# Kernel tuning notes

Measured on AMD Instinct MI355X. Metric: run time of the kernel, lower is better.

## Reference

```python
import jax, jax.numpy as jnp
import numpy as np

B, S, D, H, L, K = 16, 384, 512, 8, 4, 7
HD = D // H
MAXLEN = 400


def _pos_encoding(d=D, max_len=MAXLEN):
    # Faithful to the (unusual) torch loop: even idx i -> sin(pos/10000**(2i/d)),
    # odd idx i+1 -> cos(pos/10000**(2(i+1)/d))
    pe = np.zeros((max_len, d), dtype=np.float32)
    pos = np.arange(max_len, dtype=np.float64)[:, None]
    i = np.arange(0, d, 2)
    pe[:, i] = np.sin(pos / 10000.0 ** (2 * i / d))
    pe[:, i + 1] = np.cos(pos / 10000.0 ** (2 * (i + 1) / d))
    return jnp.asarray(pe)

POS_ENC = _pos_encoding()


def layer_norm(x, g, b, eps=1e-5):
    m = jnp.mean(x, -1, keepdims=True)
    v = jnp.mean((x - m) ** 2, -1, keepdims=True)
    return (x - m) * jax.lax.rsqrt(v + eps) * g + b


def dsconv(x, dw_w, pw_w, pw_b):
    # x: [B,S,D]; depthwise conv1d (no bias) then pointwise 1x1 (bias)
    xc = jnp.transpose(x, (0, 2, 1))  # [B,D,S]
    y = jax.lax.conv_general_dilated(
        xc, dw_w, window_strides=(1,), padding=[(K // 2, K // 2)],
        dimension_numbers=("NCH", "OIH", "NCH"), feature_group_count=D)  # [B,D,S]
    return jnp.einsum("bcs,oc->bso", y, pw_w) + pw_b  # [B,S,D]


def setup_inputs():
    key = jax.random.key(0)
    ks = jax.random.split(key, 16)
    sc = 0.02
    inp = {
        "x": jax.random.normal(ks[0], (B, S, D), jnp.float32),
        "mask": jax.random.randint(ks[1], (B, S), 0, 2, jnp.int32),
        "dw_w": jax.random.normal(ks[2], (L, D, 1, K), jnp.float32) * sc,
        "pw_w": jax.random.normal(ks[3], (L, D, D), jnp.float32) * sc,
        "pw_b": jnp.zeros((L, D), jnp.float32),
        "conv_ln_g": jnp.ones((L, D), jnp.float32),
        "conv_ln_b": jnp.zeros((L, D), jnp.float32),
        "pos_ln_g": jnp.ones((D,), jnp.float32),
        "pos_ln_b": jnp.zeros((D,), jnp.float32),
        "wq": jax.random.normal(ks[4], (D, D), jnp.float32) * sc,
        "bq": jnp.zeros((D,), jnp.float32),
        "wk": jax.random.normal(ks[5], (D, D), jnp.float32) * sc,
        "bk": jnp.zeros((D,), jnp.float32),
        "wv": jax.random.normal(ks[6], (D, D), jnp.float32) * sc,
        "bv": jnp.zeros((D,), jnp.float32),
        "wo": jax.random.normal(ks[7], (D, D), jnp.float32) * sc,
        "bo": jnp.zeros((D,), jnp.float32),
        "ff_ln_g": jnp.ones((D,), jnp.float32),
        "ff_ln_b": jnp.zeros((D,), jnp.float32),
        "ff_w": jax.random.normal(ks[8], (D, D), jnp.float32) * sc,
        "ff_b": jnp.zeros((D,), jnp.float32),
    }
    return inp


def attention(x, mask, wq, bq, wk, bk, wv, bv, wo, bo):
    def heads(w, b):
        y = jnp.einsum("bsd,od->bso", x, w) + b
        return jnp.transpose(y.reshape(B, S, H, HD), (0, 2, 1, 3))  # [B,H,S,HD]
    q, k, v = heads(wq, bq), heads(wk, bk), heads(wv, bv)
    energy = jnp.einsum("bhqd,bhkd->bhqk", q, k) / jnp.sqrt(jnp.float32(HD))
    m = (mask == 1)[:, None, None, :]  # [B,1,1,S]
    energy = jnp.where(m, jnp.float32(-1e10), energy)
    alpha = jax.nn.softmax(energy, axis=-1)  # dropout = identity (eval)
    a = jnp.einsum("bhqk,bhkd->bhqd", alpha, v)
    a = jnp.transpose(a, (0, 2, 1, 3)).reshape(B, S, D)
    return jnp.einsum("bsd,od->bso", a, wo) + bo


def reference(x, mask, dw_w, pw_w, pw_b, conv_ln_g, conv_ln_b, pos_ln_g, pos_ln_b,
              wq, bq, wk, bk, wv, bv, wo, bo, ff_ln_g, ff_ln_b, ff_w, ff_b):
    out = x + POS_ENC[None, :S, :]
    res = out
    out = layer_norm(out, pos_ln_g, pos_ln_b)
    for i in range(L):
        out = jax.nn.relu(dsconv(out, dw_w[i], pw_w[i], pw_b[i]))
        out = out + res  # dropout = identity (eval)
        res = out
        out = layer_norm(out, conv_ln_g[i], conv_ln_b[i])
    out = attention(out, mask, wq, bq, wk, bk, wv, bv, wo, bo)
    out = out + res
    res = out
    out = layer_norm(out, ff_ln_g, ff_ln_b)
    out = jax.nn.relu(jnp.einsum("bsd,od->bso", out, ff_w) + ff_b)
    return out + res
```

## Files before the change

### kernel.cpp

```cpp
#include <hip/hip_runtime.h>

#define BB 16
#define SS 384
#define DD 512
#define HH 8
#define HDIM 64
#define LLAY 4
#define KW 7
#define MM (BB*SS)

typedef unsigned short u16;
typedef unsigned int u32;
typedef short short8v __attribute__((ext_vector_type(8)));
typedef short short4v __attribute__((ext_vector_type(4)));
typedef float floatx4 __attribute__((ext_vector_type(4)));

__device__ __forceinline__ float bf2f(u16 u) {
    union { u32 i; float f; } v; v.i = ((u32)u) << 16; return v.f;
}
__device__ __forceinline__ u16 f2bf(float f) {
    union { float f; u32 i; } v; v.f = f;
    return (u16)((v.i + 0x7FFFu + ((v.i >> 16) & 1u)) >> 16);
}
__device__ __forceinline__ bool sniff_f32(const void* dtp) {
    return *((const u32*)dtp) == 0x3F800000u;
}
__device__ __forceinline__ float ldf(const void* p, long i, bool f32) {
    return f32 ? ((const float*)p)[i] : bf2f(((const u16*)p)[i]);
}
__device__ __forceinline__ short8v ldfrag_scalar(const void* p, long i, bool f32) {
    short8v r;
    if (f32) {
        const float* q = (const float*)p + i;
#pragma unroll
        for (int j = 0; j < 8; j++) r[j] = (short)f2bf(q[j]);
    } else {
        r = *(const short8v*)((const u16*)p + i);
    }
    return r;
}

__device__ __forceinline__ void load_lds16(const u16* g, u16* l) {
    __builtin_amdgcn_global_load_lds((const __attribute__((address_space(1))) void*)g,
                                     (__attribute__((address_space(3))) void*)l, 16, 0, 0);
}
__device__ __forceinline__ int swz(int row) { return (row & 3) ^ ((row >> 2) & 3); }
__device__ __forceinline__ short8v lds_frag(const u16* buf, int row, int quad) {
    return *(const short8v*)(buf + ((size_t)row * 4 + (quad ^ swz(row))) * 8);
}

#define WCV_DW 2359296
#define WCV_TOT (WCV_DW + LLAY*KW*DD)
#define NCVB ((WCV_TOT + 255) / 256)

__global__ __launch_bounds__(256) void posln_cvt_kernel(
    const void* __restrict__ x, const void* __restrict__ g, const void* __restrict__ bvec,
    u16* __restrict__ res, u16* __restrict__ out,
    const void* __restrict__ pw_w, const void* __restrict__ wq,
    const void* __restrict__ wk, const void* __restrict__ wv,
    const void* __restrict__ wo, const void* __restrict__ ff_w,
    const void* __restrict__ dw_w, u16* __restrict__ wdst,
    const void* __restrict__ dtp) {
    const bool f32 = sniff_f32(dtp);
    const int tid = threadIdx.x;
    if (blockIdx.x >= MM) {
        const int i = (blockIdx.x - MM) * 256 + tid;
        if (i >= WCV_TOT) return;
        const void* src; long idx;
        if (i < 1048576) { src = pw_w; idx = i; }
        else if (i < WCV_DW) {
            const int j = i - 1048576;
            const int m = j >> 18;
            idx = j & 262143;
            src = (m == 0) ? wq : (m == 1) ? wk : (m == 2) ? wv : (m == 3) ? wo : ff_w;
        } else {
            const int j = i - WCV_DW;
            const int l = j / (KW * DD);
            const int r1 = j % (KW * DD);
            const int t = r1 / DD, c = r1 % DD;
            src = dw_w; idx = ((long)l * DD + c) * KW + t;
        }
        wdst[i] = f2bf(ldf(src, idx, f32));
        return;
    }
    const int row = blockIdx.x;
    const int s = row % SS;
    float v[2];
#pragma unroll
    for (int i = 0; i < 2; i++) {
        const int d = tid + i * 256;
        const float freq = __expf(-(float)d * 0.035977892078032f);
        const float arg = (float)s * freq;
        const float pe = (d & 1) ? __cosf(arg) : __sinf(arg);
        v[i] = ldf(x, (long)row * DD + d, f32) + pe;
        res[row * DD + d] = f2bf(v[i]);
    }
    float sum = v[0] + v[1], sq = v[0] * v[0] + v[1] * v[1];
#pragma unroll
    for (int off = 32; off; off >>= 1) { sum += __shfl_down(sum, off); sq += __shfl_down(sq, off); }
    __shared__ float red[4][2];
    const int wv2 = tid >> 6;
    if ((tid & 63) == 0) { red[wv2][0] = sum; red[wv2][1] = sq; }
    __syncthreads();
    sum = red[0][0] + red[1][0] + red[2][0] + red[3][0];
    sq  = red[0][1] + red[1][1] + red[2][1] + red[3][1];
    const float mean = sum * (1.f / DD);
    const float rstd = rsqrtf(sq * (1.f / DD) - mean * mean + 1e-5f);
#pragma unroll
    for (int i = 0; i < 2; i++) {
        const int d = tid + i * 256;
        out[row * DD + d] = f2bf((v[i] - mean) * rstd * ldf(g, d, f32) + ldf(bvec, d, f32));
    }
}

__global__ __launch_bounds__(512) void lnres_kernel(const u16* __restrict__ y,
                                                    const void* __restrict__ g,
                                                    const void* __restrict__ bvec,
                                                    int blayer,
                                                    u16* __restrict__ out,
                                                    const void* __restrict__ dtp) {
    const bool f32 = sniff_f32(dtp);
    const long voff = (long)blayer * DD;
    const int row = blockIdx.x * 8 + (threadIdx.x >> 6);
    const int lane = threadIdx.x & 63;
    const short8v v = *(const short8v*)(y + (size_t)row * DD + lane * 8);
    float f[8], sum = 0.f, sq = 0.f;
#pragma unroll
    for (int j = 0; j < 8; j++) { f[j] = bf2f((u16)v[j]); sum += f[j]; sq += f[j] * f[j]; }
#pragma unroll
    for (int off = 32; off; off >>= 1) { sum += __shfl_xor(sum, off); sq += __shfl_xor(sq, off); }
    const float mean = sum * (1.f / DD);
    const float rstd = rsqrtf(sq * (1.f / DD) - mean * mean + 1e-5f);
    short8v o;
#pragma unroll
    for (int j = 0; j < 8; j++) {
        const int d = lane * 8 + j;
        o[j] = (short)f2bf((f[j] - mean) * rstd * ldf(g, voff + d, f32) + ldf(bvec, voff + d, f32));
    }
    *(short8v*)(out + (size_t)row * DD + lane * 8) = o;
}

template <int VEC>
__global__ __launch_bounds__(256) void dwconv_kernel(const u16* __restrict__ in,
                                                     const void* __restrict__ w, int layer,
                                                     u16* __restrict__ out,
                                                     const void* __restrict__ dtp) {
    if constexpr (VEC) {
        const int bsw = (blockIdx.x & 7) * (MM * DD / 8 / 256 / 8) + (blockIdx.x >> 3);
        const int idx = bsw * 256 + threadIdx.x;
        const int c8 = (idx & 63) * 8;
        const int ms = idx >> 6;
        const int s = ms % SS;
        const u16* wl = (const u16*)w + (size_t)layer * KW * DD;
        float acc[8] = {0, 0, 0, 0, 0, 0, 0, 0};
#pragma unroll
        for (int t = 0; t < KW; t++) {
            const int ss2 = s + t - 3;
            if (ss2 >= 0 && ss2 < SS) {
                const short8v iv = *(const short8v*)(in + (size_t)(ms + t - 3) * DD + c8);
                const short8v wv = *(const short8v*)(wl + t * DD + c8);
#pragma unroll
                for (int j = 0; j < 8; j++)
                    acc[j] += bf2f((u16)iv[j]) * bf2f((u16)wv[j]);
            }
        }
        short8v ov;
#pragma unroll
        for (int j = 0; j < 8; j++) ov[j] = (short)f2bf(acc[j]);
        *(short8v*)(out + (size_t)ms * DD + c8) = ov;
    } else {
        const bool f32 = sniff_f32(dtp);
        const long woff = (long)layer * DD * KW;
        const int idx = blockIdx.x * 256 + threadIdx.x;
        const int c = idx & (DD - 1);
        const int ms = idx >> 9;
        const int s = ms % SS;
        float acc = 0.f;
#pragma unroll
        for (int t = 0; t < KW; t++) {
            const int ss2 = s + t - 3;
            if (ss2 >= 0 && ss2 < SS)
                acc += bf2f(in[(ms + t - 3) * DD + c]) * ldf(w, woff + c * KW + t, f32);
        }
        out[idx] = f2bf(acc);
    }
}

__device__ __forceinline__ void stage64(const u16* A, const u16* Wp, int m0,
                                        u16* Ab, u16* Wb, int tid, int k0) {
#pragma unroll
    for (int j = 0; j < 2; j++) {
        const int c = j * 256 + tid;
        const int row = c >> 2;
        const int kp = (c & 3) ^ swz(row);
        load_lds16(Wp + (size_t)row * DD + k0 + kp * 8, Wb + (size_t)c * 8);
    }
    {
        const int row = tid >> 2;
        const int kp = (tid & 3) ^ swz(row);
        load_lds16(A + (size_t)(m0 + row) * DD + k0 + kp * 8, Ab + (size_t)tid * 8);
    }
}

__device__ __forceinline__ floatx4 mfma16(short8v a, short8v b, floatx4 c) {
    return __builtin_amdgcn_mfma_f32_16x16x32_bf16(a, b, c, 0, 0, 0);
}

__device__ __forceinline__ void kloop64(const u16* A, const u16* Wp, int m0,
                                        u16* Abuf, u16* Wbuf,
                                        int tid, int wm, int wn, int ln15, int quad,
                                        floatx4 acc[2][4]) {
    stage64(A, Wp, m0, Abuf, Wbuf, tid, 0);
    __syncthreads();
    for (int ks = 0; ks < 16; ks++) {
        const int cur = ks & 1;
        u16* Ab = Abuf + cur * (64 * 32);
        u16* Wb = Wbuf + cur * (128 * 32);
        if (ks < 15)
            stage64(A, Wp, m0, Abuf + (cur ^ 1) * (64 * 32),
                    Wbuf + (cur ^ 1) * (128 * 32), tid, (ks + 1) * 32);
        const short8v a0 = lds_frag(Ab, wm * 32 + ln15, quad);
        const short8v a1 = lds_frag(Ab, wm * 32 + 16 + ln15, quad);
#pragma unroll
        for (int nt = 0; nt < 4; nt++) {
            const short8v b = lds_frag(Wb, wn * 64 + nt * 16 + ln15, quad);
            acc[0][nt] = mfma16(a0, b, acc[0][nt]);
            acc[1][nt] = mfma16(a1, b, acc[1][nt]);
        }
        __syncthreads();
    }
}

template <int RELU, int FINAL>
__global__ __launch_bounds__(256, 4) void gemm64_kernel(
    const u16* __restrict__ A, const u16* __restrict__ W,
    const void* __restrict__ bias, int blayer,
    const u16* __restrict__ res_in, u16* __restrict__ res_out,
    void* __restrict__ out, const void* __restrict__ dtp) {
    const bool f32 = sniff_f32(dtp);
    const long voff = (long)blayer * DD;
    __shared__ __align__(16) u16 smem[12288];
    u16* Wbuf = smem;
    u16* Abuf = smem + 8192;
    const int tid = threadIdx.x;
    const int m0 = blockIdx.x * 64, n0 = blockIdx.y * 128;
    const int wave = tid >> 6, lane = tid & 63;
    const int wm = wave >> 1, wn = wave & 1;
    const int ln15 = lane & 15, quad = lane >> 4;

    floatx4 acc[2][4];
#pragma unroll
    for (int mt = 0; mt < 2; mt++)
#pragma unroll
        for (int nt = 0; nt < 4; nt++) acc[mt][nt] = {0.f, 0.f, 0.f, 0.f};

    kloop64(A, W + (size_t)n0 * DD, m0, Abuf, Wbuf, tid, wm, wn, ln15, quad, acc);

#pragma unroll
    for (int nt = 0; nt < 4; nt++) {
        const int col = n0 + wn * 64 + nt * 16 + ln15;
        const float bval = ldf(bias, voff + col, f32);
#pragma unroll
        for (int mt = 0; mt < 2; mt++)
#pragma unroll
            for (int r = 0; r < 4; r++) {
                const int m = m0 + wm * 32 + mt * 16 + quad * 4 + r;
                float y = acc[mt][nt][r] + bval;
                if (RELU) y = fmaxf(y, 0.f);
                y += bf2f(res_in[(size_t)m * DD + col]);
                if (res_out) res_out[(size_t)m * DD + col] = f2bf(y);
                if constexpr (FINAL) {
                    if (f32) ((float*)out)[(size_t)m * DD + col] = y;
                    else     ((u16*)out)[(size_t)m * DD + col] = f2bf(y);
                }
            }
    }
}

#define VP 72
__global__ __launch_bounds__(256, 4) void qkv64_kernel(
    const u16* __restrict__ A,
    const u16* __restrict__ Wq, const u16* __restrict__ Wk, const u16* __restrict__ Wv,
    const void* __restrict__ bq, const void* __restrict__ bk, const void* __restrict__ bv,
    u16* __restrict__ qo, u16* __restrict__ ko, u16* __restrict__ vo,
    const void* __restrict__ dtp) {
    const bool f32 = sniff_f32(dtp);
    const int sel = blockIdx.z;
    const u16* W = (sel == 0) ? Wq : (sel == 1) ? Wk : Wv;
    const void* bias = (sel == 0) ? bq : (sel == 1) ? bk : bv;

    __shared__ __align__(16) u16 smem[12288];
    u16* Wbuf = smem;
    u16* Abuf = smem + 8192;
    u16 (*vtile)[VP] = (u16 (*)[VP])smem;

    const int tid = threadIdx.x;
    const int m0 = blockIdx.x * 64, n0 = blockIdx.y * 128;
    const int wave = tid >> 6, lane = tid & 63;
    const int wm = wave >> 1, wn = wave & 1;
    const int ln15 = lane & 15, quad = lane >> 4;
    const int bidx = m0 / SS;

    floatx4 acc[2][4];
#pragma unroll
    for (int mt = 0; mt < 2; mt++)
#pragma unroll
        for (int nt = 0; nt < 4; nt++) acc[mt][nt] = {0.f, 0.f, 0.f, 0.f};

    kloop64(A, W + (size_t)n0 * DD, m0, Abuf, Wbuf, tid, wm, wn, ln15, quad, acc);

    if (sel == 2) {
#pragma unroll
        for (int nt = 0; nt < 4; nt++) {
            const int cl = wn * 64 + nt * 16 + ln15;
            const float bval = ldf(bias, n0 + cl, f32);
#pragma unroll
            for (int mt = 0; mt < 2; mt++)
#pragma unroll
                for (int r = 0; r < 4; r++)
                    vtile[cl][wm * 32 + mt * 16 + quad * 4 + r] = f2bf(acc[mt][nt][r] + bval);
        }
        __syncthreads();
        const int c = tid & 127, half = tid >> 7;
        const int col = n0 + c;
        const int h = col >> 6, hd = col & 63;
        u16* dst = vo + ((size_t)(bidx * HH + h) * HDIM + hd) * SS
                      + (m0 - bidx * SS) + half * 32;
        const u16* srcl = &vtile[c][half * 32];
#pragma unroll
        for (int j = 0; j < 4; j++)
            *(short8v*)(dst + j * 8) = *(const short8v*)(srcl + j * 8);
    } else {
        u16* out = (sel == 0) ? qo : ko;
#pragma unroll
        for (int nt = 0; nt < 4; nt++) {
            const int col = n0 + wn * 64 + nt * 16 + ln15;
            const int h = col >> 6, hd = col & 63;
            const float bval = ldf(bias, col, f32);
#pragma unroll
            for (int mt = 0; mt < 2; mt++)
#pragma unroll
                for (int r = 0; r < 4; r++) {
                    const int m = m0 + wm * 32 + mt * 16 + quad * 4 + r;
                    const int s = m - bidx * SS;
                    out[((size_t)(bidx * HH + h) * SS + s) * HDIM + hd] = f2bf(acc[mt][nt][r] + bval);
                }
        }
    }
}

template <int RELU, int DO_LN, int FINAL>
__global__ __launch_bounds__(512, 4) void gemm16_kernel(
    const u16* __restrict__ A, const void* __restrict__ W, int wlayer,
    const void* __restrict__ bias, const void* __restrict__ g,
    const void* __restrict__ bvec, int blayer,
    const u16* __restrict__ res_in, u16* __restrict__ res_out,
    void* __restrict__ out, const void* __restrict__ dtp) {
    const bool f32 = sniff_f32(dtp);
    const long woff = (long)wlayer * DD * DD;
    const long voff = (long)blayer * DD;
    __shared__ float part[8][16][2];
    const int tid = threadIdx.x;
    const int m0 = blockIdx.x * 16;
    const int wave = tid >> 6, lane = tid & 63;
    const int ln15 = lane & 15, quad = lane >> 4;

    floatx4 acc[4];
#pragma unroll
    for (int nt = 0; nt < 4; nt++) acc[nt] = {0.f, 0.f, 0.f, 0.f};

    const u16* A0 = A + (size_t)(m0 + ln15) * DD + quad * 8;
#pragma unroll
    for (int ks = 0; ks < 16; ks++) {
        const int k0 = ks * 32;
        short8v a0 = *(const short8v*)(A0 + k0);
        short8v b[4];
#pragma unroll
        for (int nt = 0; nt < 4; nt++) {
            const long wrow = woff + (long)(wave * 64 + nt * 16 + ln15) * DD + quad * 8 + k0;
            b[nt] = ldfrag_scalar(W, wrow, f32);
        }
#pragma unroll
        for (int nt = 0; nt < 4; nt++)
            acc[nt] = mfma16(a0, b[nt], acc[nt]);
    }

#pragma unroll
    for (int nt = 0; nt < 4; nt++) {
        const int col = wave * 64 + nt * 16 + ln15;
        const float bval = ldf(bias, voff + col, f32);
#pragma unroll
        for (int r = 0; r < 4; r++) {
            const int m = m0 + quad * 4 + r;
            float y = acc[nt][r] + bval;
            if (RELU) y = fmaxf(y, 0.f);
            y += bf2f(res_in[(size_t)m * DD + col]);
            if (res_out) res_out[(size_t)m * DD + col] = f2bf(y);
            acc[nt][r] = y;
        }
    }
    if constexpr (DO_LN) {
        float ls[4], lq[4];
#pragma unroll
        for (int r = 0; r < 4; r++) {
            float s = 0.f, q = 0.f;
#pragma unroll
            for (int nt = 0; nt < 4; nt++) { const float y = acc[nt][r]; s += y; q += y * y; }
            ls[r] = s; lq[r] = q;
        }
#pragma unroll
        for (int off = 1; off < 16; off <<= 1)
#pragma unroll
            for (int r = 0; r < 4; r++) {
                ls[r] += __shfl_xor(ls[r], off);
                lq[r] += __shfl_xor(lq[r], off);
            }
        if (ln15 == 0) {
#pragma unroll
            for (int r = 0; r < 4; r++) {
                part[wave][quad * 4 + r][0] = ls[r];
                part[wave][quad * 4 + r][1] = lq[r];
            }
        }
        __syncthreads();
        float mean[4], rstd[4];
#pragma unroll
        for (int r = 0; r < 4; r++) {
            const int rr = quad * 4 + r;
            float s = 0.f, q = 0.f;
#pragma unroll
            for (int wv = 0; wv < 8; wv++) { s += part[wv][rr][0]; q += part[wv][rr][1]; }
            const float mn = s * (1.f / DD);
            mean[r] = mn;
            rstd[r] = rsqrtf(q * (1.f / DD) - mn * mn + 1e-5f);
        }
#pragma unroll
        for (int nt = 0; nt < 4; nt++) {
            const int col = wave * 64 + nt * 16 + ln15;
            const float gv = ldf(g, voff + col, f32);
            const float bv = ldf(bvec, voff + col, f32);
#pragma unroll
            for (int r = 0; r < 4; r++) {
                const int m = m0 + quad * 4 + r;
                ((u16*)out)[(size_t)m * DD + col] =
                    f2bf((acc[nt][r] - mean[r]) * rstd[r] * gv + bv);
            }
        }
    } else {
#pragma unroll
        for (int nt = 0; nt < 4; nt++) {
            const int col = wave * 64 + nt * 16 + ln15;
#pragma unroll
            for (int r = 0; r < 4; r++) {
                const int m = m0 + quad * 4 + r;
                if (FINAL && f32) ((float*)out)[(size_t)m * DD + col] = acc[nt][r];
                else              ((u16*)out)[(size_t)m * DD + col] = f2bf(acc[nt][r]);
            }
        }
    }
}

__global__ __launch_bounds__(512, 4) void qkv16_kernel(
    const u16* __restrict__ A,
    const void* __restrict__ Wq, const void* __restrict__ Wk, const void* __restrict__ Wv,
    const void* __restrict__ bq, const void* __restrict__ bk, const void* __restrict__ bv,
    u16* __restrict__ qo, u16* __restrict__ ko, u16* __restrict__ vo,
    const void* __restrict__ dtp) {
    const bool f32 = sniff_f32(dtp);
    const int sel = blockIdx.y;
    const void* W = (sel == 0) ? Wq : (sel == 1) ? Wk : Wv;
    const void* bias = (sel == 0) ? bq : (sel == 1) ? bk : bv;

    const int tid = threadIdx.x;
    const int m0 = blockIdx.x * 16;
    const int wave = tid >> 6, lane = tid & 63;
    const int ln15 = lane & 15, quad = lane >> 4;
    const int bidx = m0 / SS;

    floatx4 acc[4];
#pragma unroll
    for (int nt = 0; nt < 4; nt++) acc[nt] = {0.f, 0.f, 0.f, 0.f};

    const u16* A0 = A + (size_t)(m0 + ln15) * DD + quad * 8;
#pragma unroll
    for (int ks = 0; ks < 16; ks++) {
        const int k0 = ks * 32;
        short8v a0 = *(const short8v*)(A0 + k0);
        short8v b[4];
#pragma unroll
        for (int nt = 0; nt < 4; nt++) {
            const long wrow = (long)(wave * 64 + nt * 16 + ln15) * DD + quad * 8 + k0;
            b[nt] = ldfrag_scalar(W, wrow, f32);
        }
#pragma unroll
        for (int nt = 0; nt < 4; nt++)
            acc[nt] = mfma16(a0, b[nt], acc[nt]);
    }

    if (sel == 2) {
#pragma unroll
        for (int nt = 0; nt < 4; nt++) {
            const int col = wave * 64 + nt * 16 + ln15;
            const int h = col >> 6, hd = col & 63;
            const float bval = ldf(bias, col, f32);
#pragma unroll
            for (int r = 0; r < 4; r++) {
                const int m = m0 + quad * 4 + r;
                const int s = m - bidx * SS;
                vo[((size_t)(bidx * HH + h) * HDIM + hd) * SS + s] = f2bf(acc[nt][r] + bval);
            }
        }
    } else {
        u16* out = (sel == 0) ? qo : ko;
#pragma unroll
        for (int nt = 0; nt < 4; nt++) {
            const int col = wave * 64 + nt * 16 + ln15;
            const int h = col >> 6, hd = col & 63;
            const float bval = ldf(bias, col, f32);
#pragma unroll
            for (int r = 0; r < 4; r++) {
                const int m = m0 + quad * 4 + r;
                const int s = m - bidx * SS;
                out[((size_t)(bidx * HH + h) * SS + s) * HDIM + hd] = f2bf(acc[nt][r] + bval);
            }
        }
    }
}

#define SSPF 388
#define SSPH 392
__global__ __launch_bounds__(256) void attn_kernel(const u16* __restrict__ q,
                                                   const u16* __restrict__ k,
                                                   const u16* __restrict__ vT,
                                                   const int* __restrict__ mask,
                                                   u16* __restrict__ out) {
    __shared__ float sc[16 * SSPF];
    __shared__ float rsum[16];
    u16* al = (u16*)sc;

    const int n = blockIdx.x;
    const int i = n >> 3;
    const int g = (n & 7) * 16 + i / 24;
    const int qt = i % 24;
    const int h = g & 7, b = g >> 3;
    const int q0 = qt * 16;
    const int wave = threadIdx.x >> 6, lane = threadIdx.x & 63;
    const int ln15 = lane & 15, quad = lane >> 4;

    const u16* qh = q + (size_t)(b * HH + h) * SS * HDIM;
    const u16* kh = k + (size_t)(b * HH + h) * SS * HDIM;

    const short8v* arow = (const short8v*)(qh + (q0 + ln15) * HDIM + quad * 8);
    const short8v a0 = arow[0], a1 = arow[4];
#pragma unroll
    for (int t = 0; t < 6; t++) {
        const int n0 = wave * 96 + t * 16;
        const short8v* brow = (const short8v*)(kh + (n0 + ln15) * HDIM + quad * 8);
        floatx4 acc = {0.f, 0.f, 0.f, 0.f};
        __builtin_amdgcn_s_setprio(1);
        acc = mfma16(a0, brow[0], acc);
        acc = mfma16(a1, brow[4], acc);
        __builtin_amdgcn_s_setprio(0);
        const int kk = n0 + ln15;
        const bool msk = (mask[b * SS + kk] == 1);
#pragma unroll
        for (int r = 0; r < 4; r++) {
            float v = acc[r] * 0.125f;
            if (msk) v = -1e10f;
            sc[(quad * 4 + r) * SSPF + kk] = v;
        }
    }
    __syncthreads();
    const int r = threadIdx.x >> 4, cg = threadIdx.x & 15;
    float pv[24], mx = -3.0e38f;
#pragma unroll
    for (int j = 0; j < 24; j++) { pv[j] = sc[r * SSPF + cg + 16 * j]; mx = fmaxf(mx, pv[j]); }
#pragma unroll
    for (int off = 8; off; off >>= 1) mx = fmaxf(mx, __shfl_xor(mx, off, 16));
    float sum = 0.f;
#pragma unroll
    for (int j = 0; j < 24; j++) { const float p = __expf(pv[j] - mx); pv[j] = p; sum += p; }
#pragma unroll
    for (int off = 8; off; off >>= 1) sum += __shfl_xor(sum, off, 16);
    if (cg == 0) rsum[r] = sum;
    __syncthreads();
#pragma unroll
    for (int j = 0; j < 24; j++) al[r * SSPH + cg + 16 * j] = f2bf(pv[j]);
    __syncthreads();
    const u16* vh = vT + (size_t)(b * HH + h) * HDIM * SS;
    const int d0 = wave * 16;
    floatx4 acc = {0.f, 0.f, 0.f, 0.f};
    __builtin_amdgcn_s_setprio(1);
#pragma unroll
    for (int k0 = 0; k0 < SS; k0 += 32) {
        const short8v af = *(const short8v*)(al + ln15 * SSPH + k0 + quad * 8);
        const short8v bf = *(const short8v*)(vh + (d0 + ln15) * SS + k0 + quad * 8);
        acc = mfma16(af, bf, acc);
    }
    __builtin_amdgcn_s_setprio(0);
#pragma unroll
    for (int rr = 0; rr < 4; rr++) {
        const int lr = quad * 4 + rr;
        const int s = q0 + lr;
        out[((size_t)(b * SS + s)) * DD + h * HDIM + d0 + ln15] = f2bf(acc[rr] / rsum[lr]);
    }
}

extern "C" void kernel_launch(void* const* d_in, const int* in_sizes, int n_in,
                              void* d_out, int out_size, void* d_ws, size_t ws_size,
                              hipStream_t stream) {
    (void)in_sizes; (void)n_in; (void)out_size;
    const void* x     = d_in[0];
    const int*  mask  = (const int*)d_in[1];
    const void* dw_w  = d_in[2];
    const void* pw_w  = d_in[3];
    const void* pw_b  = d_in[4];
    const void* cln_g = d_in[5];
    const void* cln_b = d_in[6];
    const void* pln_g = d_in[7];
    const void* pln_b = d_in[8];
    const void* wq    = d_in[9];
    const void* bq    = d_in[10];
    const void* wk    = d_in[11];
    const void* bk    = d_in[12];
    const void* wv    = d_in[13];
    const void* bv    = d_in[14];
    const void* wo    = d_in[15];
    const void* bo    = d_in[16];
    const void* fln_g = d_in[17];
    const void* fln_b = d_in[18];
    const void* ff_w  = d_in[19];
    const void* ff_b  = d_in[20];
    const void* dtp   = cln_g;

    const size_t nAct = (size_t)MM * DD;
    char* p = (char*)d_ws;
    u16* res   = (u16*)p; p += nAct * 2;
    u16* lnout = (u16*)p; p += nAct * 2;
    u16* tmp   = (u16*)p; p += nAct * 2;
    u16* vT    = (u16*)p; p += nAct * 2;
    u16* wcv   = (u16*)p;
    u16* kb    = (u16*)d_out;

    const size_t needFast = nAct * 2 * 4 + (size_t)WCV_TOT * 2;
    const bool fast = (ws_size >= needFast);

    if (fast) {
        posln_cvt_kernel<<<MM + NCVB, 256, 0, stream>>>(
            x, pln_g, pln_b, res, lnout,
            pw_w, wq, wk, wv, wo, ff_w, dw_w, wcv, dtp);
        const u16* w_pw = wcv;
        const u16* w_q  = wcv + 1048576;
        const u16* w_k  = wcv + 1310720;
        const u16* w_v  = wcv + 1572864;
        const u16* w_o  = wcv + 1835008;
        const u16* w_ff = wcv + 2097152;
        const u16* w_dw = wcv + WCV_DW;

        for (int i = 0; i < LLAY; i++) {
            dwconv_kernel<1><<<MM * DD / 8 / 256, 256, 0, stream>>>(lnout, w_dw, i, tmp, dtp);
            gemm64_kernel<1, 0><<<dim3(MM / 64, 4), 256, 0, stream>>>(
                tmp, w_pw + (size_t)i * DD * DD, pw_b, i, res, res, nullptr, dtp);
            lnres_kernel<<<MM / 8, 512, 0, stream>>>(res, cln_g, cln_b, i, lnout, dtp);
        }
        qkv64_kernel<<<dim3(MM / 64, 4, 3), 256, 0, stream>>>(
            lnout, w_q, w_k, w_v, bq, bk, bv, tmp, kb, vT, dtp);

        attn_kernel<<<BB * HH * (SS / 16), 256, 0, stream>>>(tmp, kb, vT, mask, lnout);

        gemm64_kernel<0, 0><<<dim3(MM / 64, 4), 256, 0, stream>>>(
            lnout, w_o, bo, 0, res, res, nullptr, dtp);
        lnres_kernel<<<MM / 8, 512, 0, stream>>>(res, fln_g, fln_b, 0, lnout, dtp);
        gemm64_kernel<1, 1><<<dim3(MM / 64, 4), 256, 0, stream>>>(
            lnout, w_ff, ff_b, 0, res, nullptr, d_out, dtp);
    } else {
        posln_cvt_kernel<<<MM, 256, 0, stream>>>(
            x, pln_g, pln_b, res, lnout,
            pw_w, wq, wk, wv, wo, ff_w, dw_w, (u16*)d_ws, dtp);
        for (int i = 0; i < LLAY; i++) {
            dwconv_kernel<0><<<MM * DD / 256, 256, 0, stream>>>(lnout, dw_w, i, tmp, dtp);
            gemm16_kernel<1, 1, 0><<<MM / 16, 512, 0, stream>>>(
                tmp, pw_w, i, pw_b, cln_g, cln_b, i, res, res, lnout, dtp);
        }
        qkv16_kernel<<<dim3(MM / 16, 3), 512, 0, stream>>>(
            lnout, wq, wk, wv, bq, bk, bv, tmp, kb, vT, dtp);

        attn_kernel<<<BB * HH * (SS / 16), 256, 0, stream>>>(tmp, kb, vT, mask, lnout);

        gemm16_kernel<0, 1, 0><<<MM / 16, 512, 0, stream>>>(
            lnout, wo, 0, bo, fln_g, fln_b, 0, res, res, lnout, dtp);
        gemm16_kernel<1, 0, 1><<<MM / 16, 512, 0, stream>>>(
            lnout, ff_w, 0, ff_b, nullptr, nullptr, 0, res, nullptr, d_out, dtp);
    }
}
```

Before: 349.4 us.

## Use 32-row GEMM tiles and per-wave 16-query attention without block syncs

Replaces the 64x128 GEMM tile with a 32x128 tile where each wave owns 32 output columns, doubling the number of blocks for the pointwise, output and FFN GEMMs. This gives more parallelism at the cost of more redundant weight loads per output. The attention kernel is restructured so each wave handles its own 16 query rows across all keys. Scores stay in registers, softmax reductions use lane shuffles, and probabilities go to a per-wave LDS slice, removing the block-wide __syncthreads and shared score buffer, with a quarter as many blocks. The trade-offs are higher register pressure (24 accumulators) and each wave rereading all of K and V.

```diff
diff --git a/kernel.cpp b/kernel.cpp
--- a/kernel.cpp
+++ b/kernel.cpp
@@ -12,7 +12,6 @@
 typedef unsigned short u16;
 typedef unsigned int u32;
 typedef short short8v __attribute__((ext_vector_type(8)));
-typedef short short4v __attribute__((ext_vector_type(4)));
 typedef float floatx4 __attribute__((ext_vector_type(4)));
 
 __device__ __forceinline__ float bf2f(u16 u) {
@@ -47,6 +46,10 @@
 __device__ __forceinline__ int swz(int row) { return (row & 3) ^ ((row >> 2) & 3); }
 __device__ __forceinline__ short8v lds_frag(const u16* buf, int row, int quad) {
     return *(const short8v*)(buf + ((size_t)row * 4 + (quad ^ swz(row))) * 8);
+}
+
+__device__ __forceinline__ floatx4 mfma16(short8v a, short8v b, floatx4 c) {
+    return __builtin_amdgcn_mfma_f32_16x16x32_bf16(a, b, c, 0, 0, 0);
 }
 
 #define WCV_DW 2359296
@@ -186,7 +189,7 @@
     }
 }
 
-__device__ __forceinline__ void stage64(const u16* A, const u16* Wp, int m0,
+__device__ __forceinline__ void stage32(const u16* A, const u16* Wp, int m0,
                                         u16* Ab, u16* Wb, int tid, int k0) {
 #pragma unroll
     for (int j = 0; j < 2; j++) {
@@ -195,15 +198,97 @@
         const int kp = (c & 3) ^ swz(row);
         load_lds16(Wp + (size_t)row * DD + k0 + kp * 8, Wb + (size_t)c * 8);
     }
+    if (tid < 128) {
+        const int row = tid >> 2;
+        const int kp = (tid & 3) ^ swz(row);
+        load_lds16(A + (size_t)(m0 + row) * DD + k0 + kp * 8, Ab + (size_t)tid * 8);
+    }
+}
+
+__device__ __forceinline__ void kloop32(const u16* A, const u16* Wp, int m0,
+                                        u16* Abuf, u16* Wbuf,
+                                        int tid, int wave, int ln15, int quad,
+                                        floatx4 acc[2][2]) {
+    stage32(A, Wp, m0, Abuf, Wbuf, tid, 0);
+    __syncthreads();
+    for (int ks = 0; ks < 16; ks++) {
+        const int cur = ks & 1;
+        u16* Ab = Abuf + cur * (32 * 32);
+        u16* Wb = Wbuf + cur * (128 * 32);
+        if (ks < 15)
+            stage32(A, Wp, m0, Abuf + (cur ^ 1) * (32 * 32),
+                    Wbuf + (cur ^ 1) * (128 * 32), tid, (ks + 1) * 32);
+        const short8v a0 = lds_frag(Ab, ln15, quad);
+        const short8v a1 = lds_frag(Ab, 16 + ln15, quad);
+#pragma unroll
+        for (int nt = 0; nt < 2; nt++) {
+            const short8v b = lds_frag(Wb, wave * 32 + nt * 16 + ln15, quad);
+            acc[0][nt] = mfma16(a0, b, acc[0][nt]);
+            acc[1][nt] = mfma16(a1, b, acc[1][nt]);
+        }
+        __syncthreads();
+    }
+}
+
+template <int RELU, int FINAL>
+__global__ __launch_bounds__(256) void gemm32w_kernel(
+    const u16* __restrict__ A, const u16* __restrict__ W,
+    const void* __restrict__ bias, int blayer,
+    const u16* __restrict__ res_in, u16* __restrict__ res_out,
+    void* __restrict__ out, const void* __restrict__ dtp) {
+    const bool f32 = sniff_f32(dtp);
+    const long voff = (long)blayer * DD;
+    __shared__ __align__(16) u16 smem[10240];
+    u16* Wbuf = smem;
+    u16* Abuf = smem + 8192;
+    const int tid = threadIdx.x;
+    const int m0 = blockIdx.x * 32, n0 = blockIdx.y * 128;
+    const int wave = tid >> 6, lane = tid & 63;
+    const int ln15 = lane & 15, quad = lane >> 4;
+
+    floatx4 acc[2][2];
+#pragma unroll
+    for (int mt = 0; mt < 2; mt++)
+#pragma unroll
+        for (int nt = 0; nt < 2; nt++) acc[mt][nt] = {0.f, 0.f, 0.f, 0.f};
+
+    kloop32(A, W + (size_t)n0 * DD, m0, Abuf, Wbuf, tid, wave, ln15, quad, acc);
+
+#pragma unroll
+    for (int nt = 0; nt < 2; nt++) {
+        const int col = n0 + wave * 32 + nt * 16 + ln15;
+        const float bval = ldf(bias, voff + col, f32);
+#pragma unroll
+        for (int mt = 0; mt < 2; mt++)
+#pragma unroll
+            for (int r = 0; r < 4; r++) {
+                const int m = m0 + mt * 16 + quad * 4 + r;
+                float y = acc[mt][nt][r] + bval;
+                if (RELU) y = fmaxf(y, 0.f);
+                y += bf2f(res_in[(size_t)m * DD + col]);
+                if (res_out) res_out[(size_t)m * DD + col] = f2bf(y);
+                if constexpr (FINAL) {
+                    if (f32) ((float*)out)[(size_t)m * DD + col] = y;
+                    else     ((u16*)out)[(size_t)m * DD + col] = f2bf(y);
+                }
+            }
+    }
+}
+
+__device__ __forceinline__ void stage64(const u16* A, const u16* Wp, int m0,
+                                        u16* Ab, u16* Wb, int tid, int k0) {
+#pragma unroll
+    for (int j = 0; j < 2; j++) {
+        const int c = j * 256 + tid;
+        const int row = c >> 2;
+        const int kp = (c & 3) ^ swz(row);
+        load_lds16(Wp + (size_t)row * DD + k0 + kp * 8, Wb + (size_t)c * 8);
+    }
     {
         const int row = tid >> 2;
         const int kp = (tid & 3) ^ swz(row);
         load_lds16(A + (size_t)(m0 + row) * DD + k0 + kp * 8, Ab + (size_t)tid * 8);
     }
-}
-
-__device__ __forceinline__ floatx4 mfma16(short8v a, short8v b, floatx4 c) {
-    return __builtin_amdgcn_mfma_f32_16x16x32_bf16(a, b, c, 0, 0, 0);
 }
 
 __device__ __forceinline__ void kloop64(const u16* A, const u16* Wp, int m0,
@@ -231,52 +316,6 @@
     }
 }
 
-template <int RELU, int FINAL>
-__global__ __launch_bounds__(256, 4) void gemm64_kernel(
-    const u16* __restrict__ A, const u16* __restrict__ W,
-    const void* __restrict__ bias, int blayer,
-    const u16* __restrict__ res_in, u16* __restrict__ res_out,
-    void* __restrict__ out, const void* __restrict__ dtp) {
-    const bool f32 = sniff_f32(dtp);
-    const long voff = (long)blayer * DD;
-    __shared__ __align__(16) u16 smem[12288];
-    u16* Wbuf = smem;
-    u16* Abuf = smem + 8192;
-    const int tid = threadIdx.x;
-    const int m0 = blockIdx.x * 64, n0 = blockIdx.y * 128;
-    const int wave = tid >> 6, lane = tid & 63;
-    const int wm = wave >> 1, wn = wave & 1;
-    const int ln15 = lane & 15, quad = lane >> 4;
-
-    floatx4 acc[2][4];
-#pragma unroll
-    for (int mt = 0; mt < 2; mt++)
-#pragma unroll
-        for (int nt = 0; nt < 4; nt++) acc[mt][nt] = {0.f, 0.f, 0.f, 0.f};
-
-    kloop64(A, W + (size_t)n0 * DD, m0, Abuf, Wbuf, tid, wm, wn, ln15, quad, acc);
-
-#pragma unroll
-    for (int nt = 0; nt < 4; nt++) {
-        const int col = n0 + wn * 64 + nt * 16 + ln15;
-        const float bval = ldf(bias, voff + col, f32);
-#pragma unroll
-        for (int mt = 0; mt < 2; mt++)
-#pragma unroll
-            for (int r = 0; r < 4; r++) {
-                const int m = m0 + wm * 32 + mt * 16 + quad * 4 + r;
-                float y = acc[mt][nt][r] + bval;
-                if (RELU) y = fmaxf(y, 0.f);
-                y += bf2f(res_in[(size_t)m * DD + col]);
-                if (res_out) res_out[(size_t)m * DD + col] = f2bf(y);
-                if constexpr (FINAL) {
-                    if (f32) ((float*)out)[(size_t)m * DD + col] = y;
-                    else     ((u16*)out)[(size_t)m * DD + col] = f2bf(y);
-                }
-            }
-    }
-}
-
 #define VP 72
 __global__ __launch_bounds__(256, 4) void qkv64_kernel(
     const u16* __restrict__ A,
@@ -527,82 +566,87 @@
     }
 }
 
-#define SSPF 388
-#define SSPH 392
+#define ALP 392
 __global__ __launch_bounds__(256) void attn_kernel(const u16* __restrict__ q,
                                                    const u16* __restrict__ k,
                                                    const u16* __restrict__ vT,
                                                    const int* __restrict__ mask,
                                                    u16* __restrict__ out) {
-    __shared__ float sc[16 * SSPF];
-    __shared__ float rsum[16];
-    u16* al = (u16*)sc;
+    __shared__ __align__(16) u16 al4[4][16][ALP];
 
     const int n = blockIdx.x;
     const int i = n >> 3;
-    const int g = (n & 7) * 16 + i / 24;
-    const int qt = i % 24;
+    const int g = (n & 7) * 16 + i / 6;
+    const int sub = i % 6;
     const int h = g & 7, b = g >> 3;
-    const int q0 = qt * 16;
     const int wave = threadIdx.x >> 6, lane = threadIdx.x & 63;
     const int ln15 = lane & 15, quad = lane >> 4;
+    const int q0 = (sub * 4 + wave) * 16;
 
     const u16* qh = q + (size_t)(b * HH + h) * SS * HDIM;
     const u16* kh = k + (size_t)(b * HH + h) * SS * HDIM;
 
     const short8v* arow = (const short8v*)(qh + (q0 + ln15) * HDIM + quad * 8);
     const short8v a0 = arow[0], a1 = arow[4];
-#pragma unroll
-    for (int t = 0; t < 6; t++) {
-        const int n0 = wave * 96 + t * 16;
-        const short8v* brow = (const short8v*)(kh + (n0 + ln15) * HDIM + quad * 8);
+
+    floatx4 sc[24];
+#pragma unroll
+    for (int t = 0; t < 24; t++) {
+        const short8v* brow = (const short8v*)(kh + (t * 16 + ln15) * HDIM + quad * 8);
         floatx4 acc = {0.f, 0.f, 0.f, 0.f};
-        __builtin_amdgcn_s_setprio(1);
         acc = mfma16(a0, brow[0], acc);
         acc = mfma16(a1, brow[4], acc);
-        __builtin_amdgcn_s_setprio(0);
-        const int kk = n0 + ln15;
-        const bool msk = (mask[b * SS + kk] == 1);
+        sc[t] = acc;
+    }
+    float mx[4] = {-3.0e38f, -3.0e38f, -3.0e38f, -3.0e38f};
+#pragma unroll
+    for (int t = 0; t < 24; t++) {
+        const bool msk = (mask[b * SS + t * 16 + ln15] == 1);
 #pragma unroll
         for (int r = 0; r < 4; r++) {
-            float v = acc[r] * 0.125f;
+            float v = sc[t][r] * 0.125f;
             if (msk) v = -1e10f;
-            sc[(quad * 4 + r) * SSPF + kk] = v;
-        }
-    }
-    __syncthreads();
-    const int r = threadIdx.x >> 4, cg = threadIdx.x & 15;
-    float pv[24], mx = -3.0e38f;
-#pragma unroll
-    for (int j = 0; j < 24; j++) { pv[j] = sc[r * SSPF + cg + 16 * j]; mx = fmaxf(mx, pv[j]); }
-#pragma unroll
-    for (int off = 8; off; off >>= 1) mx = fmaxf(mx, __shfl_xor(mx, off, 16));
-    float sum = 0.f;
-#pragma unroll
-    for (int j = 0; j < 24; j++) { const float p = __expf(pv[j] - mx); pv[j] = p; sum += p; }
-#pragma unroll
-    for (int off = 8; off; off >>= 1) sum += __shfl_xor(sum, off, 16);
-    if (cg == 0) rsum[r] = sum;
-    __syncthreads();
-#pragma unroll
-    for (int j = 0; j < 24; j++) al[r * SSPH + cg + 16 * j] = f2bf(pv[j]);
-    __syncthreads();
+            sc[t][r] = v;
+            mx[r] = fmaxf(mx[r], v);
+        }
+    }
+#pragma unroll
+    for (int off = 8; off; off >>= 1)
+#pragma unroll
+        for (int r = 0; r < 4; r++) mx[r] = fmaxf(mx[r], __shfl_xor(mx[r], off, 16));
+    float sum[4] = {0.f, 0.f, 0.f, 0.f};
+    u16* alw = &al4[wave][0][0];
+#pragma unroll
+    for (int t = 0; t < 24; t++) {
+#pragma unroll
+        for (int r = 0; r < 4; r++) {
+            const float p = __expf(sc[t][r] - mx[r]);
+            sum[r] += p;
+            alw[(quad * 4 + r) * ALP + t * 16 + ln15] = f2bf(p);
+        }
+    }
+#pragma unroll
+    for (int off = 8; off; off >>= 1)
+#pragma unroll
+        for (int r = 0; r < 4; r++) sum[r] += __shfl_xor(sum[r], off, 16);
+    __builtin_amdgcn_s_waitcnt(0);
+
     const u16* vh = vT + (size_t)(b * HH + h) * HDIM * SS;
-    const int d0 = wave * 16;
-    floatx4 acc = {0.f, 0.f, 0.f, 0.f};
-    __builtin_amdgcn_s_setprio(1);
-#pragma unroll
-    for (int k0 = 0; k0 < SS; k0 += 32) {
-        const short8v af = *(const short8v*)(al + ln15 * SSPH + k0 + quad * 8);
-        const short8v bf = *(const short8v*)(vh + (d0 + ln15) * SS + k0 + quad * 8);
-        acc = mfma16(af, bf, acc);
-    }
-    __builtin_amdgcn_s_setprio(0);
-#pragma unroll
-    for (int rr = 0; rr < 4; rr++) {
-        const int lr = quad * 4 + rr;
-        const int s = q0 + lr;
-        out[((size_t)(b * SS + s)) * DD + h * HDIM + d0 + ln15] = f2bf(acc[rr] / rsum[lr]);
+#pragma unroll
+    for (int dt = 0; dt < 4; dt++) {
+        const int d0 = dt * 16;
+        floatx4 acc = {0.f, 0.f, 0.f, 0.f};
+#pragma unroll
+        for (int k0 = 0; k0 < SS; k0 += 32) {
+            const short8v af = *(const short8v*)(alw + ln15 * ALP + k0 + quad * 8);
+            const short8v bf = *(const short8v*)(vh + (d0 + ln15) * SS + k0 + quad * 8);
+            acc = mfma16(af, bf, acc);
+        }
+#pragma unroll
+        for (int rr = 0; rr < 4; rr++) {
+            const int s = q0 + quad * 4 + rr;
+            out[((size_t)(b * SS + s)) * DD + h * HDIM + d0 + ln15] = f2bf(acc[rr] / sum[rr]);
+        }
     }
 }
 
@@ -659,19 +703,19 @@
 
         for (int i = 0; i < LLAY; i++) {
             dwconv_kernel<1><<<MM * DD / 8 / 256, 256, 0, stream>>>(lnout, w_dw, i, tmp, dtp);
-            gemm64_kernel<1, 0><<<dim3(MM / 64, 4), 256, 0, stream>>>(
+            gemm32w_kernel<1, 0><<<dim3(MM / 32, 4), 256, 0, stream>>>(
                 tmp, w_pw + (size_t)i * DD * DD, pw_b, i, res, res, nullptr, dtp);
             lnres_kernel<<<MM / 8, 512, 0, stream>>>(res, cln_g, cln_b, i, lnout, dtp);
         }
         qkv64_kernel<<<dim3(MM / 64, 4, 3), 256, 0, stream>>>(
             lnout, w_q, w_k, w_v, bq, bk, bv, tmp, kb, vT, dtp);
 
-        attn_kernel<<<BB * HH * (SS / 16), 256, 0, stream>>>(tmp, kb, vT, mask, lnout);
-
-        gemm64_kernel<0, 0><<<dim3(MM / 64, 4), 256, 0, stream>>>(
+        attn_kernel<<<BB * HH * (SS / 64), 256, 0, stream>>>(tmp, kb, vT, mask, lnout);
+
+        gemm32w_kernel<0, 0><<<dim3(MM / 32, 4), 256, 0, stream>>>(
             lnout, w_o, bo, 0, res, res, nullptr, dtp);
         lnres_kernel<<<MM / 8, 512, 0, stream>>>(res, fln_g, fln_b, 0, lnout, dtp);
-        gemm64_kernel<1, 1><<<dim3(MM / 64, 4), 256, 0, stream>>>(
+        gemm32w_kernel<1, 1><<<dim3(MM / 32, 4), 256, 0, stream>>>(
             lnout, w_ff, ff_b, 0, res, nullptr, d_out, dtp);
     } else {
         posln_cvt_kernel<<<MM, 256, 0, stream>>>(
@@ -685,7 +729,7 @@
         qkv16_kernel<<<dim3(MM / 16, 3), 512, 0, stream>>>(
             lnout, wq, wk, wv, bq, bk, bv, tmp, kb, vT, dtp);
 
-        attn_kernel<<<BB * HH * (SS / 16), 256, 0, stream>>>(tmp, kb, vT, mask, lnout);
+        attn_kernel<<<BB * HH * (SS / 64), 256, 0, stream>>>(tmp, kb, vT, mask, lnout);
 
         gemm16_kernel<0, 1, 0><<<MM / 16, 512, 0, stream>>>(
             lnout, wo, 0, bo, fln_g, fln_b, 0, res, res, lnout, dtp);
```

New measurement: 359.1 us. +2.8%, slower.
